# Kernel optimization log

Measured on AMD Instinct MI355X. Metric: run time of the kernel, lower is better.

Reference implementation:

```python
import jax, jax.numpy as jnp
import numpy as np

N, E = 50000, 800000
IN, HID, OUT, H = 128, 32, 32, 4
NEG_SLOPE = 0.2
EPS = 1e-5


def layernorm(x, g, b):
    mu = x.mean(-1, keepdims=True)
    var = ((x - mu) ** 2).mean(-1, keepdims=True)
    return (x - mu) * jax.lax.rsqrt(var + EPS) * g + b


def gat_conv(x, src, dst, W, a_s, a_d, bias, heads, ch, concat):
    n = x.shape[0]
    h = (x @ W).reshape(n, heads, ch)               # [N,H,C]
    alpha_s = (h * a_s).sum(-1)                     # [N,H]
    alpha_d = (h * a_d).sum(-1)                     # [N,H]
    e = jax.nn.leaky_relu(alpha_s[src] + alpha_d[dst], NEG_SLOPE)  # [E,H]
    m = jax.ops.segment_max(e, dst, num_segments=n)
    m = jnp.where(jnp.isfinite(m), m, 0.0)
    ex = jnp.exp(e - m[dst])
    denom = jax.ops.segment_sum(ex, dst, num_segments=n)
    alpha = ex / (denom[dst] + 1e-16)               # [E,H]
    msg = h[src] * alpha[:, :, None]                # [E,H,C]
    out = jax.ops.segment_sum(msg, dst, num_segments=n)  # [N,H,C]
    out = out.reshape(n, heads * ch) if concat else out.mean(axis=1)
    return out + bias


def setup_inputs() -> dict:
    key = jax.random.key(0)
    ks = jax.random.split(key, 24)
    HC = HID * H
    s = 0.05
    inp = {
        "x": jax.random.normal(ks[0], (N, IN), jnp.float32),
        "edge_index": jax.random.randint(ks[1], (2, E), 0, N),
        "W1": jax.random.normal(ks[2], (IN, HC), jnp.float32) * s,
        "as1": jax.random.normal(ks[3], (H, HID), jnp.float32) * s,
        "ad1": jax.random.normal(ks[4], (H, HID), jnp.float32) * s,
        "b1": jnp.zeros((HC,), jnp.float32),
        "g1": jnp.ones((HC,), jnp.float32),
        "be1": jnp.zeros((HC,), jnp.float32),
        "W2": jax.random.normal(ks[5], (HC, HC), jnp.float32) * s,
        "as2": jax.random.normal(ks[6], (H, HID), jnp.float32) * s,
        "ad2": jax.random.normal(ks[7], (H, HID), jnp.float32) * s,
        "b2": jnp.zeros((HC,), jnp.float32),
        "g2": jnp.ones((HC,), jnp.float32),
        "be2": jnp.zeros((HC,), jnp.float32),
        "W3": jax.random.normal(ks[8], (HC, OUT * H), jnp.float32) * s,
        "as3": jax.random.normal(ks[9], (H, OUT), jnp.float32) * s,
        "ad3": jax.random.normal(ks[10], (H, OUT), jnp.float32) * s,
        "b3": jnp.zeros((OUT,), jnp.float32),
        "Wsk": jax.random.normal(ks[11], (IN, HC), jnp.float32) * s,
        "bsk": jnp.zeros((HC,), jnp.float32),
    }
    return inp


def reference(x, edge_index, W1, as1, ad1, b1, g1, be1, W2, as2, ad2, b2, g2, be2, W3, as3, ad3, b3, Wsk, bsk):
    n = x.shape[0]
    loops = jnp.arange(n, dtype=edge_index.dtype)
    src = jnp.concatenate([edge_index[0], loops])
    dst = jnp.concatenate([edge_index[1], loops])
    h = gat_conv(x, src, dst, W1, as1, ad1, b1, H, HID, True)
    h = jax.nn.elu(h)
    h = layernorm(h, g1, be1)
    h = h + (x @ Wsk + bsk)  # residual (dropout is identity in eval)
    h = gat_conv(h, src, dst, W2, as2, ad2, b2, H, HID, True)
    h = jax.nn.elu(h)
    h = layernorm(h, g2, be2)
    h = gat_conv(h, src, dst, W3, as3, ad3, b3, H, OUT, False)
    return h
```

## Files before the change

kernel.cpp:

```cpp
#include <hip/hip_runtime.h>
#include <hip/hip_bf16.h>

typedef __attribute__((ext_vector_type(8))) short short8;
typedef __attribute__((ext_vector_type(4))) float f32x4;
using bf16 = __hip_bfloat16;

#define NEG_SLOPE 0.2f
#define LN_EPS 1e-5f

__device__ __forceinline__ unsigned short f2bfu(float v) {
    bf16 t = __float2bfloat16(v);
    unsigned short s;
    __builtin_memcpy(&s, &t, 2);
    return s;
}
__device__ __forceinline__ short f2bf(float v) {
    bf16 t = __float2bfloat16(v);
    short s;
    __builtin_memcpy(&s, &t, 2);
    return s;
}
__device__ __forceinline__ unsigned packbf(float a, float b) {
    return (unsigned)f2bfu(a) | ((unsigned)f2bfu(b) << 16);
}
__device__ __forceinline__ float bflo(unsigned u) { return __uint_as_float(u << 16); }
__device__ __forceinline__ float bfhi(unsigned u) { return __uint_as_float(u & 0xffff0000u); }
__device__ __forceinline__ float bf1(unsigned short u) { return __uint_as_float(((unsigned)u) << 16); }

__global__ void detect_k(const void* __restrict__ x, int* flag,
                         int* bucketCur, int CAP) {
    int lane = threadIdx.x;
    for (int i = lane; i < 512; i += 64) bucketCur[i] = i * CAP;
    const unsigned short* u = (const unsigned short*)x;
    float m = 0.f;
    for (int i = lane; i < 8192; i += 64) {
        float v = fabsf(bf1(u[i]));
        if (!(v == v)) v = 1e30f;
        m = fmaxf(m, v);
    }
    for (int d = 1; d < 64; d <<= 1) m = fmaxf(m, __shfl_xor(m, d));
    if (lane == 0) flag[0] = (m > 1e4f) ? 1 : 0;
}

struct Ptr4 { const void* p[4]; };
struct Ptr14 { const void* p[14]; };
struct Ptr3 { const void* p[3]; };
struct Ptr6 { const void* p[6]; };
__global__ void stage_k(Ptr4 Ws, bf16* __restrict__ WT,
                        Ptr14 ptrs, bf16* __restrict__ sv,
                        Ptr3 Wv, Ptr6 av, bf16* __restrict__ vaT,
                        const int* __restrict__ flag) {
    int b = blockIdx.x;
    int f = flag[0];
    if (b < 256) {
        int gid = b * 256 + threadIdx.x;
        int m = gid >> 14;
        int idx = gid & 16383;
        int i = idx >> 7, j = idx & 127;
        const void* W = Ws.p[m];
        float v = f ? ((const float*)W)[idx]
                    : __bfloat162float(((const bf16*)W)[idx]);
        WT[m * 16384 + j * 128 + i] = __float2bfloat16(v);
    } else if (b == 256) {
        for (int k = threadIdx.x; k < 14 * 128; k += 256) {
            int t = k >> 7, i = k & 127;
            int n = (t == 12) ? 32 : 128;
            if (i < n) {
                const void* s = ptrs.p[t];
                float v = f ? ((const float*)s)[i]
                            : __bfloat162float(((const bf16*)s)[i]);
                sv[k] = __float2bfloat16(v);
            }
        }
    } else {
        int gid = (b - 257) * 256 + threadIdx.x;
        int l = gid >> 11;
        if (l >= 3) return;
        int c = (gid >> 7) & 15, k = gid & 127;
        float acc = 0.f;
        if (c < 8) {
            int hd = c & 3;
            const void* W = Wv.p[l];
            const void* a = av.p[l * 2 + (c >> 2)];
            for (int j = 0; j < 32; ++j) {
                float wv = f ? ((const float*)W)[k * 128 + hd * 32 + j]
                             : __bfloat162float(((const bf16*)W)[k * 128 + hd * 32 + j]);
                float avv = f ? ((const float*)a)[hd * 32 + j]
                              : __bfloat162float(((const bf16*)a)[hd * 32 + j]);
                acc += wv * avv;
            }
        }
        vaT[gid] = __float2bfloat16(acc);
    }
}

#define SCAT_EPB 2048
__global__ __launch_bounds__(256) void bscatter_k(const int* __restrict__ src,
                                                  const int* __restrict__ dst,
                                                  int* bucketCur,
                                                  int* __restrict__ ebuf,
                                                  int E, int NB, int CAP) {
    __shared__ int lcnt[512], lbase[512];
    int t = threadIdx.x;
    int e0 = blockIdx.x * SCAT_EPB;
    int cnt = E - e0;
    if (cnt > SCAT_EPB) cnt = SCAT_EPB;
    for (int i = t; i < NB; i += 256) lcnt[i] = 0;
    __syncthreads();
    for (int i = t; i < cnt; i += 256)
        atomicAdd(&lcnt[dst[e0 + i] >> 7], 1);
    __syncthreads();
    for (int i = t; i < NB; i += 256) {
        int c = lcnt[i];
        lbase[i] = c ? atomicAdd(&bucketCur[i], c) : 0;
        lcnt[i] = 0;
    }
    __syncthreads();
    for (int i = t; i < cnt; i += 256) {
        int d = dst[e0 + i];
        int b = d >> 7;
        int pos = lbase[b] + atomicAdd(&lcnt[b], 1);
        if (pos < (b + 1) * CAP)
            ebuf[pos] = ((d & 127) << 16) | src[e0 + i];
    }
}

__global__ __launch_bounds__(256) void build_k(const int* __restrict__ ebuf,
                                               const int* __restrict__ bucketCur,
                                               int* __restrict__ rowSE,
                                               int* __restrict__ colSrc,
                                               int N, int CAP) {
    int b = blockIdx.x, t = threadIdx.x;
    int base = b * CAP;
    int cnt = bucketCur[b] - base;
    if (cnt > CAP) cnt = CAP;
    __shared__ int nodeCnt[128], nodeCur[128], ws2[2];
    if (t < 128) nodeCnt[t] = 0;
    __syncthreads();
    for (int i = t; i < cnt; i += 256)
        atomicAdd(&nodeCnt[ebuf[base + i] >> 16], 1);
    __syncthreads();
    int v = 0, incl = 0;
    if (t < 128) {
        v = nodeCnt[t];
        incl = v;
        for (int d = 1; d < 64; d <<= 1) {
            int u = __shfl_up(incl, d);
            if ((t & 63) >= d) incl += u;
        }
        if ((t & 63) == 63) ws2[t >> 6] = incl;
    }
    __syncthreads();
    if (t < 128) {
        int excl = incl - v + ((t >= 64) ? ws2[0] : 0);
        int node = b * 128 + t;
        if (node < N) {
            rowSE[node * 2] = base + excl;
            rowSE[node * 2 + 1] = base + excl + v;
        }
        nodeCur[t] = excl;
    }
    __syncthreads();
    for (int i = t; i < cnt; i += 256) {
        int p = ebuf[base + i];
        int pos = base + atomicAdd(&nodeCur[p >> 16], 1);
        colSrc[pos] = (p & 0xffff) << 8;
    }
    int capz = CAP + ((b == (int)gridDim.x - 1) ? 32 : 0);
    for (int i = cnt + t; i < capz; i += 256)
        colSrc[base + i] = 0;
}

template <int DUAL>
__global__ __launch_bounds__(256) void gemm_k(const void* __restrict__ A,
                                              const bf16* __restrict__ WT,
                                              bf16* __restrict__ out0,
                                              bf16* __restrict__ out1,
                                              const bf16* __restrict__ bias1,
                                              const bf16* __restrict__ vaT,
                                              float* __restrict__ asN,
                                              float* __restrict__ adN,
                                              int N, const int* __restrict__ flag) {
    int wave = threadIdx.x >> 6, lane = threadIdx.x & 63;
    int lm = lane & 15, lk = lane >> 4;
    const short* Ws = (const short*)WT;
    const short* Vs = (const short*)vaT;
    bool f32m = flag && flag[0];

    short8 bw0[2][4], bw1[DUAL ? 2 : 1][DUAL ? 4 : 1];
#pragma unroll
    for (int ct = 0; ct < 2; ++ct) {
        int c = (wave * 2 + ct) * 16 + lm;
#pragma unroll
        for (int kk = 0; kk < 4; ++kk)
            bw0[ct][kk] = *(const short8*)(Ws + (size_t)c * 128 + kk * 32 + lk * 8);
    }
    if (DUAL) {
#pragma unroll
        for (int ct = 0; ct < 2; ++ct) {
            int c = (wave * 2 + ct) * 16 + lm;
#pragma unroll
            for (int kk = 0; kk < 4; ++kk)
                bw1[ct][kk] = *(const short8*)(Ws + 16384 + (size_t)c * 128 + kk * 32 + lk * 8);
        }
    }
    short8 va8[4];
    if (wave == 0) {
#pragma unroll
        for (int kk = 0; kk < 4; ++kk)
            va8[kk] = *(const short8*)(Vs + (size_t)lm * 128 + kk * 32 + lk * 8);
    }
    float bv[2][4];
    if (DUAL) {
#pragma unroll
        for (int ct = 0; ct < 2; ++ct) {
            int c0 = (wave * 2 + ct) * 16 + lk * 4;
#pragma unroll
            for (int i = 0; i < 4; ++i)
                bv[ct][i] = __bfloat162float(bias1[c0 + i]);
        }
    }

    int stride = gridDim.x * 32;
    for (int rowBase = blockIdx.x * 32; rowBase < N; rowBase += stride) {
        short8 af[2][4];
#pragma unroll
        for (int rt = 0; rt < 2; ++rt) {
            int r = rowBase + rt * 16 + lm;
            if (r >= N) r = N - 1;
            if (f32m) {
#pragma unroll
                for (int kk = 0; kk < 4; ++kk) {
                    const float* Af = (const float*)A + (size_t)r * 128 + kk * 32 + lk * 8;
                    float4 q0 = *(const float4*)(Af);
                    float4 q1 = *(const float4*)(Af + 4);
                    short8 v;
                    v[0] = f2bf(q0.x); v[1] = f2bf(q0.y); v[2] = f2bf(q0.z); v[3] = f2bf(q0.w);
                    v[4] = f2bf(q1.x); v[5] = f2bf(q1.y); v[6] = f2bf(q1.z); v[7] = f2bf(q1.w);
                    af[rt][kk] = v;
                }
            } else {
#pragma unroll
                for (int kk = 0; kk < 4; ++kk)
                    af[rt][kk] = *(const short8*)((const short*)A + (size_t)r * 128 + kk * 32 + lk * 8);
            }
        }

        f32x4 acc0[2][2];
        f32x4 acc1[DUAL ? 2 : 1][DUAL ? 2 : 1];
#pragma unroll
        for (int ct = 0; ct < 2; ++ct)
#pragma unroll
            for (int rt = 0; rt < 2; ++rt) acc0[ct][rt] = (f32x4){0.f, 0.f, 0.f, 0.f};
        if (DUAL) {
#pragma unroll
            for (int ct = 0; ct < 2; ++ct)
#pragma unroll
                for (int rt = 0; rt < 2; ++rt) acc1[ct][rt] = (f32x4){0.f, 0.f, 0.f, 0.f};
        }

#pragma unroll
        for (int rt = 0; rt < 2; ++rt) {
#pragma unroll
            for (int kk = 0; kk < 4; ++kk) {
                acc0[0][rt] = __builtin_amdgcn_mfma_f32_16x16x32_bf16(bw0[0][kk], af[rt][kk], acc0[0][rt], 0, 0, 0);
                acc0[1][rt] = __builtin_amdgcn_mfma_f32_16x16x32_bf16(bw0[1][kk], af[rt][kk], acc0[1][rt], 0, 0, 0);
                if (DUAL) {
                    acc1[0][rt] = __builtin_amdgcn_mfma_f32_16x16x32_bf16(bw1[0][kk], af[rt][kk], acc1[0][rt], 0, 0, 0);
                    acc1[1][rt] = __builtin_amdgcn_mfma_f32_16x16x32_bf16(bw1[1][kk], af[rt][kk], acc1[1][rt], 0, 0, 0);
                }
            }
        }

#pragma unroll
        for (int ct = 0; ct < 2; ++ct) {
            int c0 = (wave * 2 + ct) * 16 + lk * 4;
#pragma unroll
            for (int rt = 0; rt < 2; ++rt) {
                int r = rowBase + rt * 16 + lm;
                if (r < N) {
                    uint2 pk;
                    pk.x = packbf(acc0[ct][rt][0], acc0[ct][rt][1]);
                    pk.y = packbf(acc0[ct][rt][2], acc0[ct][rt][3]);
                    *(uint2*)((unsigned short*)out0 + (size_t)r * 128 + c0) = pk;
                }
            }
        }
        if (DUAL) {
#pragma unroll
            for (int ct = 0; ct < 2; ++ct) {
                int c0 = (wave * 2 + ct) * 16 + lk * 4;
#pragma unroll
                for (int rt = 0; rt < 2; ++rt) {
                    int r = rowBase + rt * 16 + lm;
                    if (r < N) {
                        uint2 pk;
                        pk.x = packbf(acc1[ct][rt][0] + bv[ct][0], acc1[ct][rt][1] + bv[ct][1]);
                        pk.y = packbf(acc1[ct][rt][2] + bv[ct][2], acc1[ct][rt][3] + bv[ct][3]);
                        *(uint2*)((unsigned short*)out1 + (size_t)r * 128 + c0) = pk;
                    }
                }
            }
        }

        if (wave == 0) {
            f32x4 accA[2];
#pragma unroll
            for (int rt = 0; rt < 2; ++rt) accA[rt] = (f32x4){0.f, 0.f, 0.f, 0.f};
#pragma unroll
            for (int rt = 0; rt < 2; ++rt)
#pragma unroll
                for (int kk = 0; kk < 4; ++kk)
                    accA[rt] = __builtin_amdgcn_mfma_f32_16x16x32_bf16(va8[kk], af[rt][kk], accA[rt], 0, 0, 0);
            if (lk < 2) {
                float* dp = lk ? adN : asN;
#pragma unroll
                for (int rt = 0; rt < 2; ++rt) {
                    int r = rowBase + rt * 16 + lm;
                    if (r < N) *(f32x4*)(dp + (size_t)r * 4) = accA[rt];
                }
            }
        }
    }
}

template <int MODE>
__global__ __launch_bounds__(256) void agg_k(const bf16* __restrict__ h,
                                             const float* __restrict__ asN,
                                             const float* __restrict__ adN,
                                             const int* __restrict__ rowSE,
                                             const int* __restrict__ colSrc,
                                             const bf16* __restrict__ bvec,
                                             const bf16* __restrict__ g,
                                             const bf16* __restrict__ be,
                                             void* outv, int N,
                                             const int* __restrict__ flag) {
    int wv = threadIdx.x >> 6, lane = threadIdx.x & 63;
    int n = blockIdx.x * 4 + wv;
    if (n >= N) return;
    int grp = lane >> 4, t = lane & 15;
    int hd = t >> 2;
    const char* hbase = (const char*)h + t * 16;
    const char* abase = (const char*)asN + hd * 4;

    int2 se = ((const int2*)rowSE)[n];
    int st = se.x, en = se.y;
    if (en < st) en = st;

    float adn = adN[(size_t)n * 4 + hd];
    float asn_self = asN[(size_t)n * 4 + hd];
    unsigned hs = *(const unsigned*)((const char*)h + (size_t)n * 256 + t * 16 + grp * 4);

    float a[8];
#pragma unroll
    for (int k = 0; k < 8; ++k) a[k] = 0.f;
    float den = 0.f;

    int j = st + grp;
    int o0 = (j      < en) ? colSrc[j]      : 0;
    int o1 = (j + 4  < en) ? colSrc[j + 4]  : 0;
    int o2 = (j + 8  < en) ? colSrc[j + 8]  : 0;
    int o3 = (j + 12 < en) ? colSrc[j + 12] : 0;
    float av0 = *(const float*)(abase + (o0 >> 4));
    uint4 hq0 = *(const uint4*)(hbase + o0);
    float av1 = *(const float*)(abase + (o1 >> 4));
    uint4 hq1 = *(const uint4*)(hbase + o1);
    float av2 = *(const float*)(abase + (o2 >> 4));
    uint4 hq2 = *(const uint4*)(hbase + o2);
    for (; j < en; j += 4) {
        int o4 = (j + 16 < en) ? colSrc[j + 16] : 0;
        float av3 = *(const float*)(abase + (o3 >> 4));
        uint4 hq3 = *(const uint4*)(hbase + o3);
        float e = av0 + adn;
        float w = __expf(fmaxf(e, NEG_SLOPE * e));
        den += w;
        a[0] += w * bflo(hq0.x); a[1] += w * bfhi(hq0.x);
        a[2] += w * bflo(hq0.y); a[3] += w * bfhi(hq0.y);
        a[4] += w * bflo(hq0.z); a[5] += w * bfhi(hq0.z);
        a[6] += w * bflo(hq0.w); a[7] += w * bfhi(hq0.w);
        o3 = o4;
        av0 = av1; hq0 = hq1;
        av1 = av2; hq1 = hq2;
        av2 = av3; hq2 = hq3;
    }

#pragma unroll
    for (int k = 0; k < 8; ++k) {
        a[k] += __shfl_xor(a[k], 16);
        a[k] += __shfl_xor(a[k], 32);
    }
    den += __shfl_xor(den, 16);
    den += __shfl_xor(den, 32);

    float es = asn_self + adn;
    float wsf = __expf(fmaxf(es, NEG_SLOPE * es));
    den += wsf;

    float s0 = (grp & 1) ? a[2] : a[0];
    float s1 = (grp & 1) ? a[3] : a[1];
    float s2 = (grp & 1) ? a[6] : a[4];
    float s3 = (grp & 1) ? a[7] : a[5];
    float p0 = (grp & 2) ? s2 : s0;
    float p1 = (grp & 2) ? s3 : s1;

    p0 += wsf * bflo(hs);
    p1 += wsf * bfhi(hs);

    float inv = 1.f / (den + 1e-16f);
    float y0 = p0 * inv, y1 = p1 * inv;

    if (MODE == 3) {
        y0 += __shfl_xor(y0, 4); y0 += __shfl_xor(y0, 8); y0 *= 0.25f;
        y1 += __shfl_xor(y1, 4); y1 += __shfl_xor(y1, 8); y1 *= 0.25f;
        if (t < 4) {
            int oc = t * 8 + grp * 2;
            unsigned bp = *(const unsigned*)((const char*)bvec + oc * 2);
            float v0 = y0 + bflo(bp), v1 = y1 + bfhi(bp);
            if (flag[0]) {
                *(float2*)((float*)outv + (size_t)n * 32 + oc) = make_float2(v0, v1);
            } else {
                ((unsigned*)outv)[(size_t)n * 16 + (oc >> 1)] = packbf(v0, v1);
            }
        }
    } else {
        unsigned short* out = (unsigned short*)outv;
        int boff = t * 16 + grp * 4;
        unsigned bp = *(const unsigned*)((const char*)bvec + boff);
        y0 += bflo(bp); y1 += bfhi(bp);
        y0 = y0 > 0.f ? y0 : (__expf(y0) - 1.f);
        y1 = y1 > 0.f ? y1 : (__expf(y1) - 1.f);
        float s = y0 + y1, q = y0 * y0 + y1 * y1;
#pragma unroll
        for (int d = 1; d < 64; d <<= 1) {
            s += __shfl_xor(s, d);
            q += __shfl_xor(q, d);
        }
        float mu = s * (1.f / 128.f);
        float var = q * (1.f / 128.f) - mu * mu;
        var = fmaxf(var, 0.f);
        float rs = rsqrtf(var + LN_EPS);
        unsigned gp = *(const unsigned*)((const char*)g + boff);
        unsigned ep = *(const unsigned*)((const char*)be + boff);
        float z0 = (y0 - mu) * rs * bflo(gp) + bflo(ep);
        float z1 = (y1 - mu) * rs * bfhi(gp) + bfhi(ep);
        char* op = (char*)out + (size_t)n * 256 + boff;
        if (MODE == 1) {
            unsigned sk = *(const unsigned*)op;
            z0 += bflo(sk); z1 += bfhi(sk);
        }
        *(unsigned*)op = packbf(z0, z1);
    }
}

extern "C" void kernel_launch(void* const* d_in, const int* in_sizes, int n_in,
                              void* d_out, int out_size, void* d_ws, size_t ws_size,
                              hipStream_t stream) {
    const void* x  = d_in[0];
    const int*  ei = (const int*)d_in[1];

    int N = in_sizes[0] / 128;
    int E = in_sizes[1] / 2;
    const int* srcI = ei;
    const int* dstI = ei + E;

    int NB = (N + 127) >> 7;
    int CAP = (E / NB + 1024 + 511) & ~511;

    char* w = (char*)d_ws;
    size_t o = 0;
    auto carve = [&](size_t bytes) {
        void* p = w + o;
        o += (bytes + 255) & ~(size_t)255;
        return p;
    };
    int*  dtFlag = (int*)carve(256);
    bf16* WTall = (bf16*)carve(4 * 16384 * 2);
    bf16* sv   = (bf16*)carve(14 * 128 * 2);
    bf16* vaT  = (bf16*)carve(3 * 16 * 128 * 2);
    bf16* hB   = (bf16*)carve((size_t)N * 128 * 2);
    bf16* xB   = (bf16*)carve((size_t)N * 128 * 2);
    float* asN = (float*)carve((size_t)N * 4 * 4);
    float* adN = (float*)carve((size_t)N * 4 * 4);
    int* rowSE = (int*)carve((size_t)N * 2 * 4);
    int* colSrc= (int*)carve((size_t)NB * CAP * 4 + 128);
    int* ebuf  = (int*)carve((size_t)NB * CAP * 4);
    int* bucketCur = (int*)carve(512 * 4);

    detect_k<<<1, 64, 0, stream>>>(x, dtFlag, bucketCur, CAP);

    Ptr4 wp;
    wp.p[0] = d_in[2];  wp.p[1] = d_in[18];
    wp.p[2] = d_in[8];  wp.p[3] = d_in[14];
    Ptr14 ptrs;
    ptrs.p[0] = d_in[3];  ptrs.p[1] = d_in[4];  ptrs.p[2] = d_in[5];
    ptrs.p[3] = d_in[6];  ptrs.p[4] = d_in[7];
    ptrs.p[5] = d_in[9];  ptrs.p[6] = d_in[10]; ptrs.p[7] = d_in[11];
    ptrs.p[8] = d_in[12]; ptrs.p[9] = d_in[13];
    ptrs.p[10] = d_in[15]; ptrs.p[11] = d_in[16]; ptrs.p[12] = d_in[17];
    ptrs.p[13] = d_in[19];
    Ptr3 wv3;
    wv3.p[0] = d_in[2]; wv3.p[1] = d_in[8]; wv3.p[2] = d_in[14];
    Ptr6 av6;
    av6.p[0] = d_in[3];  av6.p[1] = d_in[4];
    av6.p[2] = d_in[9];  av6.p[3] = d_in[10];
    av6.p[4] = d_in[15]; av6.p[5] = d_in[16];

    stage_k<<<281, 256, 0, stream>>>(wp, WTall, ptrs, sv, wv3, av6, vaT, dtFlag);

    bscatter_k<<<(E + SCAT_EPB - 1) / SCAT_EPB, 256, 0, stream>>>(srcI, dstI,
                                                                 bucketCur, ebuf, E, NB, CAP);
    build_k<<<NB, 256, 0, stream>>>(ebuf, bucketCur, rowSE, colSrc, N, CAP);

    int gb = (N + 63) / 64;
    int nb4 = (N + 3) / 4;

    gemm_k<1><<<gb, 256, 0, stream>>>(x, WTall, hB, xB, sv + 13 * 128,
                                      vaT, asN, adN, N, dtFlag);
    agg_k<1><<<nb4, 256, 0, stream>>>(hB, asN, adN, rowSE, colSrc,
                                      sv + 2 * 128, sv + 3 * 128, sv + 4 * 128,
                                      xB, N, dtFlag);

    gemm_k<0><<<gb, 256, 0, stream>>>(xB, WTall + 2 * 16384, hB, nullptr, nullptr,
                                      vaT + 2048, asN, adN, N, nullptr);
    agg_k<2><<<nb4, 256, 0, stream>>>(hB, asN, adN, rowSE, colSrc,
                                      sv + 7 * 128, sv + 8 * 128, sv + 9 * 128,
                                      xB, N, dtFlag);

    gemm_k<0><<<gb, 256, 0, stream>>>(xB, WTall + 3 * 16384, hB, nullptr, nullptr,
                                      vaT + 4096, asN, adN, N, nullptr);
    agg_k<3><<<nb4, 256, 0, stream>>>(hB, asN, adN, rowSE, colSrc,
                                      sv + 12 * 128, nullptr, nullptr,
                                      d_out, N, dtFlag);
}
```

Baseline: 331.4 us.

## Fuse next-layer GEMM and attention projections into aggregation epilogue

The layer-2 and layer-3 linear transforms and their attention-score projections now run inside the epilogue of the previous aggregation kernel. Each block stages its four normalized node rows in shared memory and runs MFMA against weights loaded from global memory. This removes two standalone GEMM launches and the write-then-reread of the intermediate activations. The cost is that each block reloads the full weight tiles and uses only 4 of the 16 MFMA rows. Separate attention-score buffers are added so concurrent blocks do not overwrite scores that other blocks still need. The first GEMM is also de-templated to always run in dual mode.

```diff
diff --git a/kernel.cpp b/kernel.cpp
--- a/kernel.cpp
+++ b/kernel.cpp
@@ -171,7 +171,6 @@
         colSrc[base + i] = 0;
 }
 
-template <int DUAL>
 __global__ __launch_bounds__(256) void gemm_k(const void* __restrict__ A,
                                               const bf16* __restrict__ WT,
                                               bf16* __restrict__ out0,
@@ -187,21 +186,14 @@
     const short* Vs = (const short*)vaT;
     bool f32m = flag && flag[0];
 
-    short8 bw0[2][4], bw1[DUAL ? 2 : 1][DUAL ? 4 : 1];
+    short8 bw0[2][4], bw1[2][4];
 #pragma unroll
     for (int ct = 0; ct < 2; ++ct) {
         int c = (wave * 2 + ct) * 16 + lm;
 #pragma unroll
-        for (int kk = 0; kk < 4; ++kk)
+        for (int kk = 0; kk < 4; ++kk) {
             bw0[ct][kk] = *(const short8*)(Ws + (size_t)c * 128 + kk * 32 + lk * 8);
-    }
-    if (DUAL) {
-#pragma unroll
-        for (int ct = 0; ct < 2; ++ct) {
-            int c = (wave * 2 + ct) * 16 + lm;
-#pragma unroll
-            for (int kk = 0; kk < 4; ++kk)
-                bw1[ct][kk] = *(const short8*)(Ws + 16384 + (size_t)c * 128 + kk * 32 + lk * 8);
+            bw1[ct][kk] = *(const short8*)(Ws + 16384 + (size_t)c * 128 + kk * 32 + lk * 8);
         }
     }
     short8 va8[4];
@@ -211,14 +203,12 @@
             va8[kk] = *(const short8*)(Vs + (size_t)lm * 128 + kk * 32 + lk * 8);
     }
     float bv[2][4];
-    if (DUAL) {
-#pragma unroll
-        for (int ct = 0; ct < 2; ++ct) {
-            int c0 = (wave * 2 + ct) * 16 + lk * 4;
-#pragma unroll
-            for (int i = 0; i < 4; ++i)
-                bv[ct][i] = __bfloat162float(bias1[c0 + i]);
-        }
+#pragma unroll
+    for (int ct = 0; ct < 2; ++ct) {
+        int c0 = (wave * 2 + ct) * 16 + lk * 4;
+#pragma unroll
+        for (int i = 0; i < 4; ++i)
+            bv[ct][i] = __bfloat162float(bias1[c0 + i]);
     }
 
     int stride = gridDim.x * 32;
@@ -246,18 +236,14 @@
             }
         }
 
-        f32x4 acc0[2][2];
-        f32x4 acc1[DUAL ? 2 : 1][DUAL ? 2 : 1];
+        f32x4 acc0[2][2], acc1[2][2];
 #pragma unroll
         for (int ct = 0; ct < 2; ++ct)
 #pragma unroll
-            for (int rt = 0; rt < 2; ++rt) acc0[ct][rt] = (f32x4){0.f, 0.f, 0.f, 0.f};
-        if (DUAL) {
-#pragma unroll
-            for (int ct = 0; ct < 2; ++ct)
-#pragma unroll
-                for (int rt = 0; rt < 2; ++rt) acc1[ct][rt] = (f32x4){0.f, 0.f, 0.f, 0.f};
-        }
+            for (int rt = 0; rt < 2; ++rt) {
+                acc0[ct][rt] = (f32x4){0.f, 0.f, 0.f, 0.f};
+                acc1[ct][rt] = (f32x4){0.f, 0.f, 0.f, 0.f};
+            }
 
 #pragma unroll
         for (int rt = 0; rt < 2; ++rt) {
@@ -265,10 +251,8 @@
             for (int kk = 0; kk < 4; ++kk) {
                 acc0[0][rt] = __builtin_amdgcn_mfma_f32_16x16x32_bf16(bw0[0][kk], af[rt][kk], acc0[0][rt], 0, 0, 0);
                 acc0[1][rt] = __builtin_amdgcn_mfma_f32_16x16x32_bf16(bw0[1][kk], af[rt][kk], acc0[1][rt], 0, 0, 0);
-                if (DUAL) {
-                    acc1[0][rt] = __builtin_amdgcn_mfma_f32_16x16x32_bf16(bw1[0][kk], af[rt][kk], acc1[0][rt], 0, 0, 0);
-                    acc1[1][rt] = __builtin_amdgcn_mfma_f32_16x16x32_bf16(bw1[1][kk], af[rt][kk], acc1[1][rt], 0, 0, 0);
-                }
+                acc1[0][rt] = __builtin_amdgcn_mfma_f32_16x16x32_bf16(bw1[0][kk], af[rt][kk], acc1[0][rt], 0, 0, 0);
+                acc1[1][rt] = __builtin_amdgcn_mfma_f32_16x16x32_bf16(bw1[1][kk], af[rt][kk], acc1[1][rt], 0, 0, 0);
             }
         }
 
@@ -279,26 +263,13 @@
             for (int rt = 0; rt < 2; ++rt) {
                 int r = rowBase + rt * 16 + lm;
                 if (r < N) {
-                    uint2 pk;
-                    pk.x = packbf(acc0[ct][rt][0], acc0[ct][rt][1]);
-                    pk.y = packbf(acc0[ct][rt][2], acc0[ct][rt][3]);
-                    *(uint2*)((unsigned short*)out0 + (size_t)r * 128 + c0) = pk;
-                }
-            }
-        }
-        if (DUAL) {
-#pragma unroll
-            for (int ct = 0; ct < 2; ++ct) {
-                int c0 = (wave * 2 + ct) * 16 + lk * 4;
-#pragma unroll
-                for (int rt = 0; rt < 2; ++rt) {
-                    int r = rowBase + rt * 16 + lm;
-                    if (r < N) {
-                        uint2 pk;
-                        pk.x = packbf(acc1[ct][rt][0] + bv[ct][0], acc1[ct][rt][1] + bv[ct][1]);
-                        pk.y = packbf(acc1[ct][rt][2] + bv[ct][2], acc1[ct][rt][3] + bv[ct][3]);
-                        *(uint2*)((unsigned short*)out1 + (size_t)r * 128 + c0) = pk;
-                    }
+                    uint2 pk0, pk1;
+                    pk0.x = packbf(acc0[ct][rt][0], acc0[ct][rt][1]);
+                    pk0.y = packbf(acc0[ct][rt][2], acc0[ct][rt][3]);
+                    pk1.x = packbf(acc1[ct][rt][0] + bv[ct][0], acc1[ct][rt][1] + bv[ct][1]);
+                    pk1.y = packbf(acc1[ct][rt][2] + bv[ct][2], acc1[ct][rt][3] + bv[ct][3]);
+                    *(uint2*)((unsigned short*)out0 + (size_t)r * 128 + c0) = pk0;
+                    *(uint2*)((unsigned short*)out1 + (size_t)r * 128 + c0) = pk1;
                 }
             }
         }
@@ -333,11 +304,21 @@
                                              const bf16* __restrict__ bvec,
                                              const bf16* __restrict__ g,
                                              const bf16* __restrict__ be,
-                                             void* outv, int N,
+                                             void* outv,
+                                             const bf16* __restrict__ Wnext,
+                                             const bf16* __restrict__ vaNext,
+                                             bf16* __restrict__ hOut,
+                                             float* __restrict__ asOut,
+                                             float* __restrict__ adOut,
+                                             int N,
                                              const int* __restrict__ flag) {
     int wv = threadIdx.x >> 6, lane = threadIdx.x & 63;
     int n = blockIdx.x * 4 + wv;
-    if (n >= N) return;
+    if (MODE == 3) {
+        if (n >= N) return;
+    } else {
+        if (n >= N) n = N - 1;
+    }
     int grp = lane >> 4, t = lane & 15;
     int hd = t >> 2;
     const char* hbase = (const char*)h + t * 16;
@@ -423,7 +404,7 @@
             }
         }
     } else {
-        unsigned short* out = (unsigned short*)outv;
+        __shared__ short zs[4 * 128];
         int boff = t * 16 + grp * 4;
         unsigned bp = *(const unsigned*)((const char*)bvec + boff);
         y0 += bflo(bp); y1 += bfhi(bp);
@@ -443,12 +424,51 @@
         unsigned ep = *(const unsigned*)((const char*)be + boff);
         float z0 = (y0 - mu) * rs * bflo(gp) + bflo(ep);
         float z1 = (y1 - mu) * rs * bfhi(gp) + bfhi(ep);
-        char* op = (char*)out + (size_t)n * 256 + boff;
         if (MODE == 1) {
-            unsigned sk = *(const unsigned*)op;
+            unsigned sk = *(const unsigned*)((const char*)outv + (size_t)n * 256 + boff);
             z0 += bflo(sk); z1 += bfhi(sk);
         }
-        *(unsigned*)op = packbf(z0, z1);
+        *((unsigned*)zs + wv * 64 + (boff >> 2)) = packbf(z0, z1);
+        __syncthreads();
+
+        int lm = t;
+        int lk = grp;
+        const short* Wn = (const short*)Wnext;
+        short8 af[4];
+#pragma unroll
+        for (int kk = 0; kk < 4; ++kk)
+            af[kk] = *(const short8*)(zs + (lm & 3) * 128 + kk * 32 + lk * 8);
+        int nb = blockIdx.x * 4 + lm;
+#pragma unroll
+        for (int ct = 0; ct < 2; ++ct) {
+            int c = (wv * 2 + ct) * 16 + lm;
+            f32x4 acc = (f32x4){0.f, 0.f, 0.f, 0.f};
+#pragma unroll
+            for (int kk = 0; kk < 4; ++kk) {
+                short8 bw = *(const short8*)(Wn + (size_t)c * 128 + kk * 32 + lk * 8);
+                acc = __builtin_amdgcn_mfma_f32_16x16x32_bf16(bw, af[kk], acc, 0, 0, 0);
+            }
+            if (lm < 4 && nb < N) {
+                int c0 = (wv * 2 + ct) * 16 + lk * 4;
+                uint2 pk;
+                pk.x = packbf(acc[0], acc[1]);
+                pk.y = packbf(acc[2], acc[3]);
+                *(uint2*)((unsigned short*)hOut + (size_t)nb * 128 + c0) = pk;
+            }
+        }
+        if (wv == 0) {
+            const short* Vn = (const short*)vaNext;
+            f32x4 accA = (f32x4){0.f, 0.f, 0.f, 0.f};
+#pragma unroll
+            for (int kk = 0; kk < 4; ++kk) {
+                short8 va = *(const short8*)(Vn + (size_t)lm * 128 + kk * 32 + lk * 8);
+                accA = __builtin_amdgcn_mfma_f32_16x16x32_bf16(va, af[kk], accA, 0, 0, 0);
+            }
+            if (lm < 4 && lk < 2 && nb < N) {
+                float* dp = lk ? adOut : asOut;
+                *(f32x4*)(dp + (size_t)nb * 4) = accA;
+            }
+        }
     }
 }
 
@@ -481,6 +501,8 @@
     bf16* xB   = (bf16*)carve((size_t)N * 128 * 2);
     float* asN = (float*)carve((size_t)N * 4 * 4);
     float* adN = (float*)carve((size_t)N * 4 * 4);
+    float* asN2 = (float*)carve((size_t)N * 4 * 4);
+    float* adN2 = (float*)carve((size_t)N * 4 * 4);
     int* rowSE = (int*)carve((size_t)N * 2 * 4);
     int* colSrc= (int*)carve((size_t)NB * CAP * 4 + 128);
     int* ebuf  = (int*)carve((size_t)NB * CAP * 4);
@@ -514,21 +536,26 @@
     int gb = (N + 63) / 64;
     int nb4 = (N + 3) / 4;
 
-    gemm_k<1><<<gb, 256, 0, stream>>>(x, WTall, hB, xB, sv + 13 * 128,
-                                      vaT, asN, adN, N, dtFlag);
+    gemm_k<<<gb, 256, 0, stream>>>(x, WTall, hB, xB, sv + 13 * 128,
+                                   vaT, asN, adN, N, dtFlag);
+
     agg_k<1><<<nb4, 256, 0, stream>>>(hB, asN, adN, rowSE, colSrc,
                                       sv + 2 * 128, sv + 3 * 128, sv + 4 * 128,
-                                      xB, N, dtFlag);
-
-    gemm_k<0><<<gb, 256, 0, stream>>>(xB, WTall + 2 * 16384, hB, nullptr, nullptr,
-                                      vaT + 2048, asN, adN, N, nullptr);
-    agg_k<2><<<nb4, 256, 0, stream>>>(hB, asN, adN, rowSE, colSrc,
+                                      xB,
+                                      WTall + 2 * 16384, vaT + 2048,
+                                      xB, asN2, adN2,
+                                      N, dtFlag);
+
+    agg_k<2><<<nb4, 256, 0, stream>>>(xB, asN2, adN2, rowSE, colSrc,
                                       sv + 7 * 128, sv + 8 * 128, sv + 9 * 128,
-                                      xB, N, dtFlag);
-
-    gemm_k<0><<<gb, 256, 0, stream>>>(xB, WTall + 3 * 16384, hB, nullptr, nullptr,
-                                      vaT + 4096, asN, adN, N, nullptr);
+                                      nullptr,
+                                      WTall + 3 * 16384, vaT + 4096,
+                                      hB, asN, adN,
+                                      N, dtFlag);
+
     agg_k<3><<<nb4, 256, 0, stream>>>(hB, asN, adN, rowSE, colSrc,
                                       sv + 12 * 128, nullptr, nullptr,
-                                      d_out, N, dtFlag);
-}
+                                      d_out,
+                                      nullptr, nullptr, nullptr, nullptr, nullptr,
+                                      N, dtFlag);
+}
```

New measurement: 385.1 us. 1.16x slower.
